# Kernel optimization log

Measured on AMD Instinct MI355X. Metric: run time of the kernel, lower is better.

## Reference

```python
import jax, jax.numpy as jnp
import numpy as np

H = 512; W = 512; PH = 16; PW = 16; Q = 3; JITTER = 1e-06
NH = H // PH; NW = W // PW; P = NH * NW
B = 64


def setup_inputs() -> dict:
    key = jax.random.key(0)
    k0, k1, k2, k3, k4 = jax.random.split(key, 5)
    x = jax.random.normal(k0, (B, H, W), dtype=jnp.float32)
    logits = jax.random.normal(k1, (P, Q), dtype=jnp.float32)
    mu = jax.random.normal(k2, (P, Q, 2), dtype=jnp.float32) * 0.3
    sigma = jnp.exp(jax.random.normal(k3, (P, Q, 2), dtype=jnp.float32) * 0.3)
    bias = jax.random.normal(k4, (P, PH, PW), dtype=jnp.float32)
    return {"x": x, "logits": logits, "mu": mu, "sigma": sigma, "bias": bias}


def _make_S(logits, mu, sigma):
    # logits: (P,Q), mu/sigma: (P,Q,2) -> S: (P,PH,PW)
    w = jax.nn.softmax(logits, axis=-1)            # (P,Q)
    fy = jnp.fft.fftfreq(PH).astype(jnp.float32)   # (PH,)
    fx = jnp.fft.fftfreq(PW).astype(jnp.float32)   # (PW,)
    mu_y = mu[..., 0][:, :, None, None]            # (P,Q,1,1)
    mu_x = mu[..., 1][:, :, None, None]
    sg_y = sigma[..., 0][:, :, None, None]
    sg_x = sigma[..., 1][:, :, None, None]
    fy_b = fy[None, None, :, None]                 # (1,1,PH,1)
    fx_b = fx[None, None, None, :]                 # (1,1,1,PW)
    g1 = jnp.exp(-0.5 * (((fy_b - mu_y) / sg_y) ** 2 + ((fx_b - mu_x) / sg_x) ** 2))
    g2 = jnp.exp(-0.5 * (((fy_b + mu_y) / sg_y) ** 2 + ((fx_b + mu_x) / sg_x) ** 2))
    # weighted sum over mixture components Q
    S = jnp.einsum('pq,pqhw->phw', w, g1 + g2) + JITTER
    return S


def reference(x, logits, mu, sigma, bias):
    # x: (B,H,W) -> (B,H,W)
    S = _make_S(logits, mu, sigma)                                  # (P,PH,PW)
    x_p = x.reshape(B, NH, PH, NW, PW)
    x_p = x_p.transpose(1, 3, 0, 2, 4).reshape(P, B, PH, PW)        # (P,B,PH,PW)
    Xf = jnp.fft.fftn(x_p, axes=(-2, -1))                           # complex64
    y_p = jnp.fft.ifftn(Xf * S[:, None, :, :], axes=(-2, -1)).real  # (P,B,PH,PW)
    y_p = y_p + bias[:, None, :, :]
    y = y_p.reshape(NH, NW, B, PH, PW)
    y = y.transpose(2, 0, 3, 1, 4).reshape(B, H, W)
    return y
```

## Files before the change

kernel.cpp:

```cpp
#include <hip/hip_runtime.h>
#include <math.h>

#define HH 512
#define WW 512
#define PHH 16
#define PWW 16
#define QQ 3
#define NHH 32
#define NWW 32
#define PP 1024
#define BB 64

__device__ __constant__ float TWC[8] = {
    1.0f,  0.92387953251f,  0.70710678119f,  0.38268343236f,
    0.0f, -0.38268343236f, -0.70710678119f, -0.92387953251f};
__device__ __constant__ float TWS[8] = {
    0.0f, -0.38268343236f, -0.70710678119f, -0.92387953251f,
   -1.0f, -0.92387953251f, -0.70710678119f, -0.38268343236f};

template <int SGN>
__device__ __forceinline__ void fft16(float* re, float* im) {
#define SWAP_(a, b)                              \
  { float t = re[a]; re[a] = re[b]; re[b] = t;   \
    t = im[a]; im[a] = im[b]; im[b] = t; }
  SWAP_(1, 8) SWAP_(2, 4) SWAP_(3, 12) SWAP_(5, 10) SWAP_(7, 14) SWAP_(11, 13)
#undef SWAP_
#pragma unroll
  for (int len = 2; len <= 16; len <<= 1) {
    const int half = len >> 1;
    const int tstep = 16 / len;
#pragma unroll
    for (int i = 0; i < 16; i += len) {
#pragma unroll
      for (int j = 0; j < half; ++j) {
        const float wr = TWC[j * tstep];
        const float wi = (SGN > 0) ? TWS[j * tstep] : -TWS[j * tstep];
        const int a = i + j;
        const int c = i + j + half;
        const float tr = re[c] * wr - im[c] * wi;
        const float ti = re[c] * wi + im[c] * wr;
        re[c] = re[a] - tr;
        im[c] = im[a] - ti;
        re[a] = re[a] + tr;
        im[a] = im[a] + ti;
      }
    }
  }
}

__global__ __launch_bounds__(256) void psm_kernel(
    const float* __restrict__ x, const float* __restrict__ logits,
    const float* __restrict__ mu, const float* __restrict__ sigma,
    const float* __restrict__ bias, float* __restrict__ out) {
  __shared__ float S_lds[256];
  __shared__ float t_re[16 * 272];
  __shared__ float t_im[16 * 272];

  const int tid = threadIdx.x;
  const int p = blockIdx.x >> 2;
  const int b0 = (blockIdx.x & 3) << 4;
  const int g = tid >> 4;
  const int r = tid & 15;
  const int b = b0 + g;
  const int nh = p >> 5;
  const int nw = p & 31;

  {
    const int fy_i = tid >> 4;
    const int fx_i = tid & 15;
    const float fy = (float)(fy_i < 8 ? fy_i : fy_i - 16) * (1.0f / 16.0f);
    const float fx = (float)(fx_i < 8 ? fx_i : fx_i - 16) * (1.0f / 16.0f);
    const float l0 = logits[p * QQ + 0];
    const float l1 = logits[p * QQ + 1];
    const float l2 = logits[p * QQ + 2];
    const float lm = fmaxf(l0, fmaxf(l1, l2));
    const float e0 = __expf(l0 - lm);
    const float e1 = __expf(l1 - lm);
    const float e2 = __expf(l2 - lm);
    const float inv = 1.0f / (e0 + e1 + e2);
    const float wq[3] = {e0 * inv, e1 * inv, e2 * inv};
    float s = 0.0f;
#pragma unroll
    for (int q = 0; q < QQ; ++q) {
      const float muy = mu[(p * QQ + q) * 2 + 0];
      const float mux = mu[(p * QQ + q) * 2 + 1];
      const float isy = 1.0f / sigma[(p * QQ + q) * 2 + 0];
      const float isx = 1.0f / sigma[(p * QQ + q) * 2 + 1];
      const float dy1 = (fy - muy) * isy;
      const float dx1 = (fx - mux) * isx;
      const float dy2 = (fy + muy) * isy;
      const float dx2 = (fx + mux) * isx;
      const float g1 = __expf(-0.5f * (dy1 * dy1 + dx1 * dx1));
      const float g2 = __expf(-0.5f * (dy2 * dy2 + dx2 * dx2));
      s += wq[q] * (g1 + g2);
    }
    S_lds[tid] = (s + 1e-6f) * (1.0f / 256.0f);
  }
  __syncthreads();

  const size_t rowoff =
      (size_t)b * (HH * WW) + (size_t)(nh * PHH + r) * WW + (size_t)(nw * PWW);
  const float* xrow = x + rowoff;
  float re[16], im[16];
#pragma unroll
  for (int c4 = 0; c4 < 4; ++c4) {
    const float4 v = ((const float4*)xrow)[c4];
    re[c4 * 4 + 0] = v.x;
    re[c4 * 4 + 1] = v.y;
    re[c4 * 4 + 2] = v.z;
    re[c4 * 4 + 3] = v.w;
  }
#pragma unroll
  for (int c = 0; c < 16; ++c) im[c] = 0.0f;

  fft16<1>(re, im);

  float* mre = &t_re[g * 272];
  float* mim = &t_im[g * 272];
#pragma unroll
  for (int c = 0; c < 16; ++c) {
    mre[r * 17 + c] = re[c];
    mim[r * 17 + c] = im[c];
  }
  __syncthreads();
#pragma unroll
  for (int k = 0; k < 16; ++k) {
    re[k] = mre[k * 17 + r];
    im[k] = mim[k * 17 + r];
  }
  __syncthreads();

  fft16<1>(re, im);
#pragma unroll
  for (int k = 0; k < 16; ++k) {
    const float s = S_lds[k * 16 + r];
    re[k] *= s;
    im[k] *= s;
  }
  fft16<-1>(re, im);

#pragma unroll
  for (int k = 0; k < 16; ++k) {
    mre[k * 17 + r] = re[k];
    mim[k * 17 + r] = im[k];
  }
  __syncthreads();
#pragma unroll
  for (int c = 0; c < 16; ++c) {
    re[c] = mre[r * 17 + c];
    im[c] = mim[r * 17 + c];
  }

  fft16<-1>(re, im);

  const float* brow = bias + (size_t)p * 256 + (size_t)r * 16;
  float* orow = out + rowoff;
#pragma unroll
  for (int c4 = 0; c4 < 4; ++c4) {
    const float4 bv = ((const float4*)brow)[c4];
    float4 o;
    o.x = re[c4 * 4 + 0] + bv.x;
    o.y = re[c4 * 4 + 1] + bv.y;
    o.z = re[c4 * 4 + 2] + bv.z;
    o.w = re[c4 * 4 + 3] + bv.w;
    ((float4*)orow)[c4] = o;
  }
}

extern "C" void kernel_launch(void* const* d_in, const int* in_sizes, int n_in,
                              void* d_out, int out_size, void* d_ws,
                              size_t ws_size, hipStream_t stream) {
  (void)in_sizes;
  (void)n_in;
  (void)out_size;
  (void)d_ws;
  (void)ws_size;
  const float* x = (const float*)d_in[0];
  const float* logits = (const float*)d_in[1];
  const float* mu = (const float*)d_in[2];
  const float* sigma = (const float*)d_in[3];
  const float* bias = (const float*)d_in[4];
  float* out = (float*)d_out;

  psm_kernel<<<dim3(PP * 4), dim3(256), 0, stream>>>(x, logits, mu, sigma,
                                                     bias, out);
}
```

Measured before the change: 147.7 us.

## Specialize FFT twiddles, drop block barriers for wave-sync LDS transposes, nontemporal I/O

The 16-point FFT now uses compile-time-specialized butterflies, so trivial twiddles (1, -i, the sqrt(1/2) cases) become adds and swaps instead of constant-memory loads and full complex multiplies. The LDS transposes no longer use __syncthreads. They rely on each 16-thread group sitting inside one 64-wide wavefront, with only compiler scheduling fences between phases, and they reuse a single buffer for real and imaginary parts, which halves LDS use. Global x loads and output stores become nontemporal, and launch bounds request higher occupancy. The barrier-free transpose depends on wavefront lockstep execution and would break if the group-to-wave mapping changed.

After: 243.3 us. 1.65x slower.

```diff
diff --git a/kernel.cpp b/kernel.cpp
--- a/kernel.cpp
+++ b/kernel.cpp
@@ -11,50 +11,78 @@
 #define PP 1024
 #define BB 64
 
-__device__ __constant__ float TWC[8] = {
-    1.0f,  0.92387953251f,  0.70710678119f,  0.38268343236f,
-    0.0f, -0.38268343236f, -0.70710678119f, -0.92387953251f};
-__device__ __constant__ float TWS[8] = {
-    0.0f, -0.38268343236f, -0.70710678119f, -0.92387953251f,
-   -1.0f, -0.92387953251f, -0.70710678119f, -0.38268343236f};
+typedef float floatx4 __attribute__((ext_vector_type(4)));
+
+__device__ __forceinline__ void wfence() {
+  asm volatile("" ::: "memory");
+  __builtin_amdgcn_sched_barrier(0);
+}
+
+template <int SGN, int T>
+__device__ __forceinline__ void bfly(float& ar, float& ai, float& br, float& bi) {
+  float tr, ti;
+  if constexpr (T == 0) {
+    tr = br;
+    ti = bi;
+  } else if constexpr (T == 4) {
+    if constexpr (SGN > 0) { tr = bi;  ti = -br; }
+    else                   { tr = -bi; ti = br;  }
+  } else if constexpr (T == 2) {
+    constexpr float c = 0.70710678118654752440f;
+    if constexpr (SGN > 0) { tr = c * (br + bi); ti = c * (bi - br); }
+    else                   { tr = c * (br - bi); ti = c * (bi + br); }
+  } else if constexpr (T == 6) {
+    constexpr float c = 0.70710678118654752440f;
+    if constexpr (SGN > 0) { tr = c * (bi - br);  ti = -c * (br + bi); }
+    else                   { tr = -c * (br + bi); ti = c * (br - bi);  }
+  } else {
+    constexpr float KC[8] = {1.0f,  0.92387953251128675613f,  0.70710678118654752440f,
+                             0.38268343236508977173f,  0.0f, -0.38268343236508977173f,
+                            -0.70710678118654752440f, -0.92387953251128675613f};
+    constexpr float KS[8] = {0.0f, -0.38268343236508977173f, -0.70710678118654752440f,
+                            -0.92387953251128675613f, -1.0f, -0.92387953251128675613f,
+                            -0.70710678118654752440f, -0.92387953251128675613f >= 0 ? -0.92387953251128675613f : -0.92387953251128675613f};
+    constexpr float wr = KC[T];
+    constexpr float wi0 = (T == 1) ? -0.38268343236508977173f
+                        : (T == 3) ? -0.92387953251128675613f
+                        : (T == 5) ? -0.92387953251128675613f
+                        : (T == 7) ? -0.38268343236508977173f
+                                   : KS[T];
+    constexpr float wi = (SGN > 0) ? wi0 : -wi0;
+    tr = br * wr - bi * wi;
+    ti = br * wi + bi * wr;
+  }
+  br = ar - tr;
+  bi = ai - ti;
+  ar = ar + tr;
+  ai = ai + ti;
+}
 
 template <int SGN>
-__device__ __forceinline__ void fft16(float* re, float* im) {
-#define SWAP_(a, b)                              \
-  { float t = re[a]; re[a] = re[b]; re[b] = t;   \
+__device__ __forceinline__ void fft16(float re[16], float im[16]) {
+#define SW_(a, b)                              \
+  { float t = re[a]; re[a] = re[b]; re[b] = t; \
     t = im[a]; im[a] = im[b]; im[b] = t; }
-  SWAP_(1, 8) SWAP_(2, 4) SWAP_(3, 12) SWAP_(5, 10) SWAP_(7, 14) SWAP_(11, 13)
-#undef SWAP_
-#pragma unroll
-  for (int len = 2; len <= 16; len <<= 1) {
-    const int half = len >> 1;
-    const int tstep = 16 / len;
-#pragma unroll
-    for (int i = 0; i < 16; i += len) {
-#pragma unroll
-      for (int j = 0; j < half; ++j) {
-        const float wr = TWC[j * tstep];
-        const float wi = (SGN > 0) ? TWS[j * tstep] : -TWS[j * tstep];
-        const int a = i + j;
-        const int c = i + j + half;
-        const float tr = re[c] * wr - im[c] * wi;
-        const float ti = re[c] * wi + im[c] * wr;
-        re[c] = re[a] - tr;
-        im[c] = im[a] - ti;
-        re[a] = re[a] + tr;
-        im[a] = im[a] + ti;
-      }
-    }
-  }
-}
-
-__global__ __launch_bounds__(256) void psm_kernel(
+  SW_(1, 8) SW_(2, 4) SW_(3, 12) SW_(5, 10) SW_(7, 14) SW_(11, 13)
+#undef SW_
+#define BF_(a, b, T) bfly<SGN, T>(re[a], im[a], re[b], im[b]);
+  BF_(0, 1, 0) BF_(2, 3, 0) BF_(4, 5, 0) BF_(6, 7, 0)
+  BF_(8, 9, 0) BF_(10, 11, 0) BF_(12, 13, 0) BF_(14, 15, 0)
+  BF_(0, 2, 0) BF_(1, 3, 4) BF_(4, 6, 0) BF_(5, 7, 4)
+  BF_(8, 10, 0) BF_(9, 11, 4) BF_(12, 14, 0) BF_(13, 15, 4)
+  BF_(0, 4, 0) BF_(1, 5, 2) BF_(2, 6, 4) BF_(3, 7, 6)
+  BF_(8, 12, 0) BF_(9, 13, 2) BF_(10, 14, 4) BF_(11, 15, 6)
+  BF_(0, 8, 0) BF_(1, 9, 1) BF_(2, 10, 2) BF_(3, 11, 3)
+  BF_(4, 12, 4) BF_(5, 13, 5) BF_(6, 14, 6) BF_(7, 15, 7)
+#undef BF_
+}
+
+__global__ __launch_bounds__(256, 8) void psm_kernel(
     const float* __restrict__ x, const float* __restrict__ logits,
     const float* __restrict__ mu, const float* __restrict__ sigma,
     const float* __restrict__ bias, float* __restrict__ out) {
   __shared__ float S_lds[256];
-  __shared__ float t_re[16 * 272];
-  __shared__ float t_im[16 * 272];
+  __shared__ float tbuf[16 * 272];
 
   const int tid = threadIdx.x;
   const int p = blockIdx.x >> 2;
@@ -104,7 +132,7 @@
   float re[16], im[16];
 #pragma unroll
   for (int c4 = 0; c4 < 4; ++c4) {
-    const float4 v = ((const float4*)xrow)[c4];
+    const floatx4 v = __builtin_nontemporal_load(((const floatx4*)xrow) + c4);
     re[c4 * 4 + 0] = v.x;
     re[c4 * 4 + 1] = v.y;
     re[c4 * 4 + 2] = v.z;
@@ -115,20 +143,19 @@
 
   fft16<1>(re, im);
 
-  float* mre = &t_re[g * 272];
-  float* mim = &t_im[g * 272];
-#pragma unroll
-  for (int c = 0; c < 16; ++c) {
-    mre[r * 17 + c] = re[c];
-    mim[r * 17 + c] = im[c];
-  }
-  __syncthreads();
-#pragma unroll
-  for (int k = 0; k < 16; ++k) {
-    re[k] = mre[k * 17 + r];
-    im[k] = mim[k * 17 + r];
-  }
-  __syncthreads();
+  float* m = &tbuf[g * 272];
+#pragma unroll
+  for (int c = 0; c < 16; ++c) m[r * 17 + c] = re[c];
+  wfence();
+#pragma unroll
+  for (int k = 0; k < 16; ++k) re[k] = m[k * 17 + r];
+  wfence();
+#pragma unroll
+  for (int c = 0; c < 16; ++c) m[r * 17 + c] = im[c];
+  wfence();
+#pragma unroll
+  for (int k = 0; k < 16; ++k) im[k] = m[k * 17 + r];
+  wfence();
 
   fft16<1>(re, im);
 #pragma unroll
@@ -140,16 +167,16 @@
   fft16<-1>(re, im);
 
 #pragma unroll
-  for (int k = 0; k < 16; ++k) {
-    mre[k * 17 + r] = re[k];
-    mim[k * 17 + r] = im[k];
-  }
-  __syncthreads();
-#pragma unroll
-  for (int c = 0; c < 16; ++c) {
-    re[c] = mre[r * 17 + c];
-    im[c] = mim[r * 17 + c];
-  }
+  for (int k = 0; k < 16; ++k) m[k * 17 + r] = re[k];
+  wfence();
+#pragma unroll
+  for (int c = 0; c < 16; ++c) re[c] = m[r * 17 + c];
+  wfence();
+#pragma unroll
+  for (int k = 0; k < 16; ++k) m[k * 17 + r] = im[k];
+  wfence();
+#pragma unroll
+  for (int c = 0; c < 16; ++c) im[c] = m[r * 17 + c];
 
   fft16<-1>(re, im);
 
@@ -157,13 +184,13 @@
   float* orow = out + rowoff;
 #pragma unroll
   for (int c4 = 0; c4 < 4; ++c4) {
-    const float4 bv = ((const float4*)brow)[c4];
-    float4 o;
+    const floatx4 bv = ((const floatx4*)brow)[c4];
+    floatx4 o;
     o.x = re[c4 * 4 + 0] + bv.x;
     o.y = re[c4 * 4 + 1] + bv.y;
     o.z = re[c4 * 4 + 2] + bv.z;
     o.w = re[c4 * 4 + 3] + bv.w;
-    ((float4*)orow)[c4] = o;
+    __builtin_nontemporal_store(o, ((floatx4*)orow) + c4);
   }
 }
 
```
